# Performance work log

Measured on AMD Instinct MI355X. Metric: run time of the kernel, lower is better.

The kernel has to match this reference:

```python
import jax, jax.numpy as jnp
import numpy as np

B = 8192        # number of contexts
T_SIDE = 10     # num_cx_tokens_per_side
NT = 10         # cx_max_num_types
V_TOK = 5000
V_TYP = 5000
D_TOK = 128
D_TYP = 32
H = 32          # hole_rnn_layer_size
D_IN = D_TOK + D_TYP  # 160


def setup_inputs() -> dict:
    key = jax.random.key(0)
    ks = jax.random.split(key, 32)
    def n(k, shape, scale=1.0):
        return jax.random.normal(k, shape, dtype=jnp.float32) * scale
    def rmask(k, shape):
        m = jax.random.randint(k, shape, 0, 2).astype(bool)
        return m.at[:, :, 0].set(True)  # first type slot always valid (as in data loader)
    inp = {}
    inp['tokens_before'] = jax.random.randint(ks[0], (B, T_SIDE), 0, V_TOK, dtype=jnp.int32)
    inp['types_before'] = jax.random.randint(ks[1], (B, T_SIDE, NT), 0, V_TYP, dtype=jnp.int32)
    inp['mask_before'] = rmask(ks[2], (B, T_SIDE, NT))
    inp['tokens_after'] = jax.random.randint(ks[3], (B, T_SIDE), 0, V_TOK, dtype=jnp.int32)
    inp['types_after'] = jax.random.randint(ks[4], (B, T_SIDE, NT), 0, V_TYP, dtype=jnp.int32)
    inp['mask_after'] = rmask(ks[5], (B, T_SIDE, NT))
    inp['token_embeddings'] = n(ks[6], (V_TOK, D_TOK))
    inp['type_embeddings'] = n(ks[7], (V_TYP, D_TYP))
    inp['hole_representation'] = n(ks[8], (1, 1, D_IN))
    # GRU kernels (TF GRUCell layout): gate kernel [(in+h), 2h], candidate [(in+h), h]
    i = 9
    for layer, din in ((0, D_IN), (1, 2 * H)):
        for d in ('fw', 'bw'):
            inp[f'gk_{d}{layer}'] = n(ks[i], (din + H, 2 * H), 0.1); i += 1
            inp[f'gb_{d}{layer}'] = jnp.zeros((2 * H,), jnp.float32)
            inp[f'ck_{d}{layer}'] = n(ks[i], (din + H, H), 0.1); i += 1
            inp[f'cb_{d}{layer}'] = jnp.zeros((H,), jnp.float32)
    return inp


def _embed(tokens, types, mask, tok_emb, typ_emb):
    te = tok_emb[tokens]                                 # [B,T,128]
    ty = typ_emb[types]                                  # [B,T,NT,32]
    ty = ty + (1.0 - mask[..., None].astype(jnp.float32)) * -1000.0
    ty = jnp.max(ty, axis=2)                             # masked max over types -> [B,T,32]
    return jnp.concatenate([te, ty], axis=-1)            # [B,T,160]


def _gru(x_seq, gk, gb, ck, cb):
    # x_seq: [T,B,D]; TF GRUCell math: r,u = sigmoid([x,h]Wg+bg); c = tanh([x, r*h]Wc+bc); h' = u*h+(1-u)*c
    h0 = jnp.zeros((x_seq.shape[1], cb.shape[0]), x_seq.dtype)
    def step(h, x):
        ru = jax.nn.sigmoid(jnp.concatenate([x, h], -1) @ gk + gb)
        r, u = jnp.split(ru, 2, axis=-1)
        c = jnp.tanh(jnp.concatenate([x, r * h], -1) @ ck + cb)
        h_new = u * h + (1.0 - u) * c
        return h_new, h_new
    _, ys = jax.lax.scan(step, h0, x_seq)
    return ys                                            # [T,B,H]


def _bidir(x_seq, pf, pb):
    fw = _gru(x_seq, *pf)
    bw = jnp.flip(_gru(jnp.flip(x_seq, 0), *pb), 0)
    return jnp.concatenate([fw, bw], axis=-1)            # [T,B,2H]


def reference(tokens_before, types_before, mask_before, tokens_after, types_after, mask_after,
              token_embeddings, type_embeddings, hole_representation,
              gk_fw0, gb_fw0, ck_fw0, cb_fw0, gk_bw0, gb_bw0, ck_bw0, cb_bw0,
              gk_fw1, gb_fw1, ck_fw1, cb_fw1, gk_bw1, gb_bw1, ck_bw1, cb_bw1):
    before = _embed(tokens_before, types_before, mask_before, token_embeddings, type_embeddings)
    after = _embed(tokens_after, types_after, mask_after, token_embeddings, type_embeddings)
    nb = before.shape[0]
    hole = jnp.broadcast_to(hole_representation, (nb, 1, D_IN))
    seq = jnp.concatenate([before, hole, after], axis=1)  # [B,21,160]
    x = jnp.transpose(seq, (1, 0, 2))                     # [T,B,D]
    y0 = _bidir(x, (gk_fw0, gb_fw0, ck_fw0, cb_fw0), (gk_bw0, gb_bw0, ck_bw0, cb_bw0))
    y1 = _bidir(y0, (gk_fw1, gb_fw1, ck_fw1, cb_fw1), (gk_bw1, gb_bw1, ck_bw1, cb_bw1))
    return jnp.transpose(y1, (1, 0, 2))                   # [B,21,64]
```

## Files before the change

kernel.cpp:

```cpp
#include <hip/hip_runtime.h>


typedef __attribute__((ext_vector_type(8))) short short8;
typedef __attribute__((ext_vector_type(8))) __bf16 bf16x8;
typedef __attribute__((ext_vector_type(4))) float f32x4;
typedef unsigned short ushort_t;

#define U_TOKEMB  0
#define U_TYPEMB  640000
#define U_HOLE    800000
#define U_GKFW0   800160
#define U_GBFW0   812448
#define U_CKFW0   812512
#define U_CBFW0   818656
#define U_GKBW0   818688
#define U_GBBW0   830976
#define U_CKBW0   831040
#define U_CBBW0   837184
#define U_GKFW1   837216
#define U_GBFW1   843360
#define U_CKFW1   843424
#define U_CBFW1   846496
#define U_GKBW1   846528
#define U_GBBW1   852672
#define U_CKBW1   852736
#define U_CBBW1   855808

#define Y0A_OFF   (4u << 20)
#define TYPF_OFF  (25u << 20)
#define WF_OFF    (37u << 20)

__device__ __forceinline__ float bf2f(unsigned int u) {
  union { unsigned int i; float f; } v; v.i = u << 16; return v.f;
}
__device__ __forceinline__ unsigned short f2bf(float f) {
  unsigned int u = __float_as_uint(f);
  u += 0x7fffu + ((u >> 16) & 1u);
  return (unsigned short)(u >> 16);
}
__device__ __forceinline__ unsigned cvtpk(float a, float b) {
  unsigned r;
  asm("v_cvt_pk_bf16_f32 %0, %1, %2" : "=v"(r) : "v"(a), "v"(b));
  return r;
}
__device__ __forceinline__ f32x4 mfma16(short8 a, short8 b, f32x4 c) {
  return __builtin_amdgcn_mfma_f32_16x16x32_bf16(
      __builtin_bit_cast(bf16x8, a), __builtin_bit_cast(bf16x8, b), c, 0, 0, 0);
}
__device__ __forceinline__ float frcp(float x) { return __builtin_amdgcn_rcpf(x); }
__device__ __forceinline__ float sgm(float x) {
  return frcp(1.f + __expf(-x));
}
__device__ __forceinline__ float tnh(float x) {
  return 1.f - 2.f * frcp(__expf(2.f * x) + 1.f);
}
__device__ __forceinline__ int PIk(int p) { return (p >> 1) + ((p & 1) << 4); }

__global__ void k0_detect(const ushort_t* __restrict__ probe_f,
                          const unsigned* __restrict__ probe_m,
                          const unsigned* __restrict__ probe_t,
                          int* __restrict__ flags) {
  const int lane = threadIdx.x;
  int cnt = 0;
#pragma unroll
  for (int i = 0; i < 4; ++i) {
    unsigned e = ((unsigned)probe_f[lane + i * 64] >> 7) & 0xffu;
    if (e == 0u || (e >= 112u && e <= 134u)) cnt++;
  }
#pragma unroll
  for (int off = 32; off > 0; off >>= 1) cnt += __shfl_down(cnt, off, 64);
  const unsigned v = probe_m[lane];
  const unsigned long long bytelike =
      __ballot((v > 1u) && (v != 0x3F800000u) && ((v & 0xFEFEFEFEu) == 0u));
  const unsigned tv = probe_t[lane];
  const unsigned long long tlooksTypes =
      __ballot(!(tv == 0u || tv == 1u || tv == 0x3F800000u));
  if (lane == 0) {
    flags[0] = (cnt < 205) ? 1 : 0;
    flags[1] = bytelike ? 1 : 0;
    flags[2] = tlooksTypes ? 0 : 1;
  }
}

struct Cvt19 { const void* src[19]; int len[19]; int dst[19]; };

__global__ void kcvt(Cvt19 a, ushort_t* __restrict__ cvt, const int* __restrict__ flags) {
  const int fp32 = flags[0];
  int gid = blockIdx.x * blockDim.x + threadIdx.x;
#pragma unroll 1
  for (int s = 0; s < 19; ++s) {
    if (gid < a.len[s]) {
      cvt[a.dst[s] + gid] = fp32 ? f2bf(((const float*)a.src[s])[gid])
                                 : ((const ushort_t*)a.src[s])[gid];
      return;
    }
    gid -= a.len[s];
  }
}

__global__ void kswz(const ushort_t* __restrict__ cvt, uint4* __restrict__ wf) {
  const int id = blockIdx.x * blockDim.x + threadIdx.x;
  if (id >= 108 * 64) return;
  const int frag = id >> 6, lane = id & 63;
  const int q = lane >> 4, nl = lane & 15;
  const int layer = (frag >= 72) ? 1 : 0;
  const int fr = layer ? frag - 72 : frag;
  const int nper = layer ? 18 : 36;
  const int d = fr / nper;
  const int f = fr - d * nper;
  const ushort_t* gk = layer ? (cvt + (d ? U_GKBW1 : U_GKFW1))
                             : (cvt + (d ? U_GKBW0 : U_GKFW0));
  const ushort_t* ck = layer ? (cvt + (d ? U_CKBW1 : U_CKFW1))
                             : (cvt + (d ? U_CKBW0 : U_CKFW0));
  const ushort_t* src; int row0, colw, coloff; bool perm;
  if (!layer) {
    if (f < 20)      { src = gk; row0 = (f >> 2) * 32; colw = 64; coloff = (f & 3) * 16; perm = false; }
    else if (f < 30) { int g = f - 20; src = ck; row0 = (g >> 1) * 32; colw = 32; coloff = (g & 1) * 16; perm = false; }
    else if (f < 34) { src = gk; row0 = 160; colw = 64; coloff = (f - 30) * 16; perm = true; }
    else             { src = ck; row0 = 160; colw = 32; coloff = (f - 34) * 16; perm = true; }
  } else {
    perm = true;
    if (f < 12)      { src = gk; row0 = (f >> 2) * 32; colw = 64; coloff = (f & 3) * 16; }
    else             { int g = f - 12; src = ck; row0 = (g >> 1) * 32; colw = 32; coloff = (g & 1) * 16; }
  }
  short8 v;
#pragma unroll
  for (int j = 0; j < 8; ++j) {
    const int p = q * 8 + j;
    const int row = row0 + (perm ? PIk(p) : p);
    v[j] = (short)src[row * colw + coloff + nl];
  }
  wf[frag * 64 + lane] = __builtin_bit_cast(uint4, v);
}

__global__ __launch_bounds__(256) void ktypmax(
    const void* __restrict__ slot_tb, const void* __restrict__ slot_mb,
    const void* __restrict__ slot_ta, const void* __restrict__ slot_ma,
    const ushort_t* __restrict__ cvt, uint4* __restrict__ typf,
    const int* __restrict__ flags) {
  const int wv = threadIdx.x >> 6;
  const int lane = threadIdx.x & 63;
  const int q = lane >> 4, nl = lane & 15;
  const int job = blockIdx.x * 4 + wv;
  const int st = job >> 9;
  const int btile = job & 511;
  const int side = (st >= 10) ? 1 : 0;
  const int ts = st - side * 10;
  const int b = btile * 16 + nl;
  const int sw = flags[2];
  const int bytem = flags[1];
  const int* tys = side ? (const int*)(sw ? slot_ma : slot_ta)
                        : (const int*)(sw ? slot_mb : slot_tb);
  const void* msk = side ? (sw ? slot_ta : slot_ma)
                         : (sw ? slot_tb : slot_mb);
  const int base = (b * 10 + ts) * 10;
  float mx[8];
#pragma unroll
  for (int j = 0; j < 8; ++j) mx[j] = -1e30f;
#pragma unroll
  for (int nt = 0; nt < 10; ++nt) {
    const int ty = tys[base + nt];
    const bool mv = bytem ? (((const unsigned char*)msk)[base + nt] != 0)
                          : (((const unsigned*)msk)[base + nt] != 0u);
    const float pen = mv ? 0.f : -1000.f;
    uint4 e = *reinterpret_cast<const uint4*>(cvt + U_TYPEMB + (size_t)ty * 32 + q * 8);
    const unsigned w[4] = {e.x, e.y, e.z, e.w};
#pragma unroll
    for (int j2 = 0; j2 < 4; ++j2) {
      mx[2 * j2]     = fmaxf(mx[2 * j2],     bf2f(w[j2] & 0xffffu) + pen);
      mx[2 * j2 + 1] = fmaxf(mx[2 * j2 + 1], bf2f(w[j2] >> 16) + pen);
    }
  }
  short8 v;
#pragma unroll
  for (int j = 0; j < 8; ++j) v[j] = (short)f2bf(mx[j]);
  typf[(size_t)job * 64 + lane] = __builtin_bit_cast(uint4, v);
}

__device__ __forceinline__ void gatherX(
    int t, int btile, int lane,
    const int* __restrict__ tok_b, const int* __restrict__ tok_a,
    const ushort_t* __restrict__ cvt, const uint4* __restrict__ typf,
    short8 af[5]) {
  const int q = lane >> 4, nl = lane & 15;
  if (t == 10) {
#pragma unroll
    for (int kt = 0; kt < 5; ++kt)
      af[kt] = __builtin_bit_cast(short8,
          *reinterpret_cast<const uint4*>(cvt + U_HOLE + kt * 32 + q * 8));
    return;
  }
  const int ts = (t < 10) ? t : t - 11;
  const int side = (t < 10) ? 0 : 1;
  const int b = btile * 16 + nl;
  const int tok = (side ? tok_a : tok_b)[b * 10 + ts];
#pragma unroll
  for (int kt = 0; kt < 4; ++kt)
    af[kt] = __builtin_bit_cast(short8,
        *reinterpret_cast<const uint4*>(cvt + U_TOKEMB + (size_t)tok * 128 + kt * 32 + q * 8));
  af[4] = __builtin_bit_cast(short8,
      typf[((size_t)(side * 10 + ts) * 512 + btile) * 64 + lane]);
}

__global__ __launch_bounds__(256, 1) void krec0(
    const int* __restrict__ tok_b, const int* __restrict__ tok_a,
    const ushort_t* __restrict__ cvt, const uint4* __restrict__ wf,
    const uint4* __restrict__ typf, uint4* __restrict__ y0a) {
  __shared__ __align__(16) ushort_t hbuf[4][2][16 * 40];
  const int wv = threadIdx.x >> 6;
  const int lane = threadIdx.x & 63;
  const int q = lane >> 4, nl = lane & 15;
  const int job = blockIdx.x * 4 + wv;
  const int dir = job & 1, btile = job >> 1;

  const uint4* wfL0 = wf + dir * 36 * 64;
  short8 wg[5][4], wc[5][2], wgh[4], wch[2];
#pragma unroll
  for (int kt = 0; kt < 5; ++kt) {
#pragma unroll
    for (int tn = 0; tn < 4; ++tn)
      wg[kt][tn] = __builtin_bit_cast(short8, wfL0[(kt * 4 + tn) * 64 + lane]);
#pragma unroll
    for (int tn = 0; tn < 2; ++tn)
      wc[kt][tn] = __builtin_bit_cast(short8, wfL0[(20 + kt * 2 + tn) * 64 + lane]);
  }
#pragma unroll
  for (int tn = 0; tn < 4; ++tn)
    wgh[tn] = __builtin_bit_cast(short8, wfL0[(30 + tn) * 64 + lane]);
#pragma unroll
  for (int tn = 0; tn < 2; ++tn)
    wch[tn] = __builtin_bit_cast(short8, wfL0[(34 + tn) * 64 + lane]);

  const ushort_t* gb = cvt + (dir ? U_GBBW0 : U_GBFW0);
  const ushort_t* cb = cvt + (dir ? U_CBBW0 : U_CBFW0);
  float gb4[4], cb4[2];
#pragma unroll
  for (int tn = 0; tn < 4; ++tn) gb4[tn] = bf2f((unsigned)gb[tn * 16 + nl]);
#pragma unroll
  for (int tn = 0; tn < 2; ++tn) cb4[tn] = bf2f((unsigned)cb[tn * 16 + nl]);

  f32x4 hc0 = {0.f, 0.f, 0.f, 0.f}, hc1 = {0.f, 0.f, 0.f, 0.f};
  short8 hA = {0, 0, 0, 0, 0, 0, 0, 0};
  ushort_t* hb0 = hbuf[wv][0];
  ushort_t* hb1 = hbuf[wv][1];

  short8 afc[5], afn[5];
  gatherX(dir ? 20 : 0, btile, lane, tok_b, tok_a, cvt, typf, afc);

  for (int s = 0; s < 21; ++s) {
    const int t = dir ? 20 - s : s;
    if (s < 20)
      gatherX(dir ? t - 1 : t + 1, btile, lane, tok_b, tok_a, cvt, typf, afn);

    f32x4 ru[4];
#pragma unroll
    for (int tn = 0; tn < 4; ++tn) {
      f32x4 acc = {gb4[tn], gb4[tn], gb4[tn], gb4[tn]};
#pragma unroll
      for (int kt = 0; kt < 5; ++kt) acc = mfma16(afc[kt], wg[kt][tn], acc);
      acc = mfma16(hA, wgh[tn], acc);
      ru[tn] = acc;
    }
#pragma unroll
    for (int tn = 0; tn < 4; ++tn)
#pragma unroll
      for (int r = 0; r < 4; ++r) ru[tn][r] = sgm(ru[tn][r]);

#pragma unroll
    for (int r = 0; r < 4; ++r)
      *reinterpret_cast<unsigned*>(hb0 + (q * 4 + r) * 40 + 2 * nl) =
          cvtpk(ru[0][r] * hc0[r], ru[1][r] * hc1[r]);
    short8 rhA = *reinterpret_cast<const short8*>(hb0 + nl * 40 + q * 8);

    f32x4 cc0 = {cb4[0], cb4[0], cb4[0], cb4[0]};
    f32x4 cc1 = {cb4[1], cb4[1], cb4[1], cb4[1]};
#pragma unroll
    for (int kt = 0; kt < 5; ++kt) {
      cc0 = mfma16(afc[kt], wc[kt][0], cc0);
      cc1 = mfma16(afc[kt], wc[kt][1], cc1);
    }
    cc0 = mfma16(rhA, wch[0], cc0);
    cc1 = mfma16(rhA, wch[1], cc1);
#pragma unroll
    for (int r = 0; r < 4; ++r) {
      const float c0 = tnh(cc0[r]), c1 = tnh(cc1[r]);
      const float u0 = ru[2][r], u1 = ru[3][r];
      hc0[r] = u0 * hc0[r] + (1.f - u0) * c0;
      hc1[r] = u1 * hc1[r] + (1.f - u1) * c1;
    }

#pragma unroll
    for (int r = 0; r < 4; ++r)
      *reinterpret_cast<unsigned*>(hb1 + (q * 4 + r) * 40 + 2 * nl) =
          cvtpk(hc0[r], hc1[r]);
    hA = *reinterpret_cast<const short8*>(hb1 + nl * 40 + q * 8);
    y0a[((size_t)(t * 512 + btile) * 2 + dir) * 64 + lane] = __builtin_bit_cast(uint4, hA);

    if (s < 20) {
#pragma unroll
      for (int kt = 0; kt < 5; ++kt) afc[kt] = afn[kt];
    }
  }
}

__global__ __launch_bounds__(256, 1) void k3b(
    const ushort_t* __restrict__ cvt, const uint4* __restrict__ wf,
    const uint4* __restrict__ y0a, float* __restrict__ out) {
  __shared__ __align__(16) ushort_t hbuf[4][2][16 * 40];
  const int wv = threadIdx.x >> 6;
  const int lane = threadIdx.x & 63;
  const int q = lane >> 4, nl = lane & 15;
  const int job = blockIdx.x * 4 + wv;
  const int dir = job & 1, btile = job >> 1;

  const uint4* wfL1 = wf + (72 + dir * 18) * 64;
  short8 wg[3][4], wc[3][2];
#pragma unroll
  for (int kt = 0; kt < 3; ++kt) {
#pragma unroll
    for (int tn = 0; tn < 4; ++tn)
      wg[kt][tn] = __builtin_bit_cast(short8, wfL1[(kt * 4 + tn) * 64 + lane]);
#pragma unroll
    for (int tn = 0; tn < 2; ++tn)
      wc[kt][tn] = __builtin_bit_cast(short8, wfL1[(12 + kt * 2 + tn) * 64 + lane]);
  }
  const ushort_t* gb = cvt + (dir ? U_GBBW1 : U_GBFW1);
  const ushort_t* cb = cvt + (dir ? U_CBBW1 : U_CBFW1);
  float gb4[4], cb4[2];
#pragma unroll
  for (int tn = 0; tn < 4; ++tn) gb4[tn] = bf2f((unsigned)gb[tn * 16 + nl]);
#pragma unroll
  for (int tn = 0; tn < 2; ++tn) cb4[tn] = bf2f((unsigned)cb[tn * 16 + nl]);

  f32x4 hc0 = {0.f, 0.f, 0.f, 0.f}, hc1 = {0.f, 0.f, 0.f, 0.f};
  short8 hA = {0, 0, 0, 0, 0, 0, 0, 0};
  ushort_t* hb0 = hbuf[wv][0];
  ushort_t* hb1 = hbuf[wv][1];

  short8 ya0, ya1, yn0, yn1;
  {
    const int t0 = dir ? 20 : 0;
    ya0 = __builtin_bit_cast(short8, y0a[((size_t)(t0 * 512 + btile) * 2 + 0) * 64 + lane]);
    ya1 = __builtin_bit_cast(short8, y0a[((size_t)(t0 * 512 + btile) * 2 + 1) * 64 + lane]);
  }

  for (int s = 0; s < 21; ++s) {
    const int t = dir ? 20 - s : s;
    if (s < 20) {
      const int t2 = dir ? t - 1 : t + 1;
      yn0 = __builtin_bit_cast(short8, y0a[((size_t)(t2 * 512 + btile) * 2 + 0) * 64 + lane]);
      yn1 = __builtin_bit_cast(short8, y0a[((size_t)(t2 * 512 + btile) * 2 + 1) * 64 + lane]);
    }

    f32x4 ru[4];
#pragma unroll
    for (int tn = 0; tn < 4; ++tn) {
      f32x4 acc = {gb4[tn], gb4[tn], gb4[tn], gb4[tn]};
      acc = mfma16(ya0, wg[0][tn], acc);
      acc = mfma16(ya1, wg[1][tn], acc);
      acc = mfma16(hA,  wg[2][tn], acc);
      ru[tn] = acc;
    }
#pragma unroll
    for (int tn = 0; tn < 4; ++tn)
#pragma unroll
      for (int r = 0; r < 4; ++r) ru[tn][r] = sgm(ru[tn][r]);

#pragma unroll
    for (int r = 0; r < 4; ++r)
      *reinterpret_cast<unsigned*>(hb0 + (q * 4 + r) * 40 + 2 * nl) =
          cvtpk(ru[0][r] * hc0[r], ru[1][r] * hc1[r]);
    short8 rhA = *reinterpret_cast<const short8*>(hb0 + nl * 40 + q * 8);

    f32x4 cc0 = {cb4[0], cb4[0], cb4[0], cb4[0]};
    cc0 = mfma16(ya0, wc[0][0], cc0);
    cc0 = mfma16(ya1, wc[1][0], cc0);
    cc0 = mfma16(rhA, wc[2][0], cc0);
    f32x4 cc1 = {cb4[1], cb4[1], cb4[1], cb4[1]};
    cc1 = mfma16(ya0, wc[0][1], cc1);
    cc1 = mfma16(ya1, wc[1][1], cc1);
    cc1 = mfma16(rhA, wc[2][1], cc1);

#pragma unroll
    for (int r = 0; r < 4; ++r) {
      const float c0 = tnh(cc0[r]), c1 = tnh(cc1[r]);
      const float u0 = ru[2][r], u1 = ru[3][r];
      hc0[r] = u0 * hc0[r] + (1.f - u0) * c0;
      hc1[r] = u1 * hc1[r] + (1.f - u1) * c1;
    }

#pragma unroll
    for (int r = 0; r < 4; ++r)
      *reinterpret_cast<unsigned*>(hb1 + (q * 4 + r) * 40 + 2 * nl) =
          cvtpk(hc0[r], hc1[r]);
    hA = *reinterpret_cast<const short8*>(hb1 + nl * 40 + q * 8);

#pragma unroll
    for (int r = 0; r < 4; ++r) {
      const size_t o = ((size_t)(btile * 16 + q * 4 + r) * 21 + t) * 64 + dir * 32 + nl;
      out[o]      = hc0[r];
      out[o + 16] = hc1[r];
    }

    if (s < 20) { ya0 = yn0; ya1 = yn1; }
  }
}

extern "C" void kernel_launch(void* const* d_in, const int* in_sizes, int n_in,
                              void* d_out, int out_size, void* d_ws, size_t ws_size,
                              hipStream_t stream)
{
  const int* tok_b = (const int*)d_in[0];
  const void* slot_tb = d_in[1];
  const void* slot_mb = d_in[2];
  const int* tok_a = (const int*)d_in[3];
  const void* slot_ta = d_in[4];
  const void* slot_ma = d_in[5];

  int* flags = (int*)d_ws;
  ushort_t* cvt = (ushort_t*)((char*)d_ws + 64);
  uint4* y0a = (uint4*)((char*)d_ws + Y0A_OFF);
  uint4* typf = (uint4*)((char*)d_ws + TYPF_OFF);
  uint4* wf  = (uint4*)((char*)d_ws + WF_OFF);

  k0_detect<<<dim3(1), dim3(64), 0, stream>>>(
      (const ushort_t*)d_in[6], (const unsigned*)slot_mb, (const unsigned*)slot_tb,
      flags);

  static const int slen[19] = {640000, 160000, 160,
                               12288, 64, 6144, 32, 12288, 64, 6144, 32,
                               6144, 64, 3072, 32, 6144, 64, 3072, 32};
  static const int sdst[19] = {U_TOKEMB, U_TYPEMB, U_HOLE,
                               U_GKFW0, U_GBFW0, U_CKFW0, U_CBFW0,
                               U_GKBW0, U_GBBW0, U_CKBW0, U_CBBW0,
                               U_GKFW1, U_GBFW1, U_CKFW1, U_CBFW1,
                               U_GKBW1, U_GBBW1, U_CKBW1, U_CBBW1};
  Cvt19 a;
  int tot = 0;
  for (int i = 0; i < 19; ++i) {
    a.src[i] = d_in[6 + i]; a.len[i] = slen[i]; a.dst[i] = sdst[i]; tot += slen[i];
  }
  kcvt<<<dim3((tot + 255) / 256), dim3(256), 0, stream>>>(a, cvt, flags);

  kswz<<<dim3(27), dim3(256), 0, stream>>>(cvt, wf);

  ktypmax<<<dim3(2560), dim3(256), 0, stream>>>(
      slot_tb, slot_mb, slot_ta, slot_ma, cvt, typf, flags);

  krec0<<<dim3(256), dim3(256), 0, stream>>>(tok_b, tok_a, cvt, wf, typf, y0a);

  k3b<<<dim3(256), dim3(256), 0, stream>>>(cvt, wf, y0a, (float*)d_out);
}
```

Baseline: 188.1 us.

## Software-pipeline GRU input projections one step ahead of the recurrence

In both GRU layer kernels, the input-side MFMA products (x·W for gates and candidate) for step t+1 are now computed during step t, interleaved with the recurrent critical path. The recurrence then only needs the single h·W MFMA per output tile, which shortens the serial dependency chain each step. Input gathers/loads move two steps ahead. This raises register pressure (extra px/pxn accumulators) and may cause spills at launch bounds 256,1.

New measurement: 193.2 us. 1.03x slower.

```diff
diff --git a/kernel.cpp b/kernel.cpp
--- a/kernel.cpp
+++ b/kernel.cpp
@@ -244,23 +244,44 @@
   ushort_t* hb0 = hbuf[wv][0];
   ushort_t* hb1 = hbuf[wv][1];
 
-  short8 afc[5], afn[5];
-  gatherX(dir ? 20 : 0, btile, lane, tok_b, tok_a, cvt, typf, afc);
+  short8 afc[5];
+  f32x4 px[6], pxn[6];
+  {
+    gatherX(dir ? 20 : 0, btile, lane, tok_b, tok_a, cvt, typf, afc);
+#pragma unroll
+    for (int tn = 0; tn < 4; ++tn) {
+      f32x4 acc = {gb4[tn], gb4[tn], gb4[tn], gb4[tn]};
+#pragma unroll
+      for (int kt = 0; kt < 5; ++kt) acc = mfma16(afc[kt], wg[kt][tn], acc);
+      px[tn] = acc;
+    }
+#pragma unroll
+    for (int tn = 0; tn < 2; ++tn) {
+      f32x4 acc = {cb4[tn], cb4[tn], cb4[tn], cb4[tn]};
+#pragma unroll
+      for (int kt = 0; kt < 5; ++kt) acc = mfma16(afc[kt], wc[kt][tn], acc);
+      px[4 + tn] = acc;
+    }
+    gatherX(dir ? 19 : 1, btile, lane, tok_b, tok_a, cvt, typf, afc);
+  }
 
   for (int s = 0; s < 21; ++s) {
     const int t = dir ? 20 - s : s;
-    if (s < 20)
-      gatherX(dir ? t - 1 : t + 1, btile, lane, tok_b, tok_a, cvt, typf, afn);
 
     f32x4 ru[4];
 #pragma unroll
-    for (int tn = 0; tn < 4; ++tn) {
-      f32x4 acc = {gb4[tn], gb4[tn], gb4[tn], gb4[tn]};
-#pragma unroll
-      for (int kt = 0; kt < 5; ++kt) acc = mfma16(afc[kt], wg[kt][tn], acc);
-      acc = mfma16(hA, wgh[tn], acc);
-      ru[tn] = acc;
-    }
+    for (int tn = 0; tn < 4; ++tn) ru[tn] = mfma16(hA, wgh[tn], px[tn]);
+
+    if (s < 20) {
+#pragma unroll
+      for (int tn = 0; tn < 4; ++tn) {
+        f32x4 acc = {gb4[tn], gb4[tn], gb4[tn], gb4[tn]};
+#pragma unroll
+        for (int kt = 0; kt < 5; ++kt) acc = mfma16(afc[kt], wg[kt][tn], acc);
+        pxn[tn] = acc;
+      }
+    }
+
 #pragma unroll
     for (int tn = 0; tn < 4; ++tn)
 #pragma unroll
@@ -272,15 +293,19 @@
           cvtpk(ru[0][r] * hc0[r], ru[1][r] * hc1[r]);
     short8 rhA = *reinterpret_cast<const short8*>(hb0 + nl * 40 + q * 8);
 
-    f32x4 cc0 = {cb4[0], cb4[0], cb4[0], cb4[0]};
-    f32x4 cc1 = {cb4[1], cb4[1], cb4[1], cb4[1]};
-#pragma unroll
-    for (int kt = 0; kt < 5; ++kt) {
-      cc0 = mfma16(afc[kt], wc[kt][0], cc0);
-      cc1 = mfma16(afc[kt], wc[kt][1], cc1);
-    }
-    cc0 = mfma16(rhA, wch[0], cc0);
-    cc1 = mfma16(rhA, wch[1], cc1);
+    f32x4 cc0 = mfma16(rhA, wch[0], px[4]);
+    f32x4 cc1 = mfma16(rhA, wch[1], px[5]);
+
+    if (s < 20) {
+#pragma unroll
+      for (int tn = 0; tn < 2; ++tn) {
+        f32x4 acc = {cb4[tn], cb4[tn], cb4[tn], cb4[tn]};
+#pragma unroll
+        for (int kt = 0; kt < 5; ++kt) acc = mfma16(afc[kt], wc[kt][tn], acc);
+        pxn[4 + tn] = acc;
+      }
+    }
+
 #pragma unroll
     for (int r = 0; r < 4; ++r) {
       const float c0 = tnh(cc0[r]), c1 = tnh(cc1[r]);
@@ -298,7 +323,9 @@
 
     if (s < 20) {
 #pragma unroll
-      for (int kt = 0; kt < 5; ++kt) afc[kt] = afn[kt];
+      for (int tn = 0; tn < 6; ++tn) px[tn] = pxn[tn];
+      if (s < 19)
+        gatherX(dir ? t - 2 : t + 2, btile, lane, tok_b, tok_a, cvt, typf, afc);
     }
   }
 }
@@ -337,30 +364,52 @@
   ushort_t* hb0 = hbuf[wv][0];
   ushort_t* hb1 = hbuf[wv][1];
 
-  short8 ya0, ya1, yn0, yn1;
+#define LOAD_YA(tt, d0, d1)                                                      \
+  do {                                                                           \
+    d0 = __builtin_bit_cast(short8,                                              \
+        y0a[((size_t)((tt) * 512 + btile) * 2 + 0) * 64 + lane]);                \
+    d1 = __builtin_bit_cast(short8,                                              \
+        y0a[((size_t)((tt) * 512 + btile) * 2 + 1) * 64 + lane]);                \
+  } while (0)
+
+  short8 ya0, ya1;
+  f32x4 px[6], pxn[6];
   {
-    const int t0 = dir ? 20 : 0;
-    ya0 = __builtin_bit_cast(short8, y0a[((size_t)(t0 * 512 + btile) * 2 + 0) * 64 + lane]);
-    ya1 = __builtin_bit_cast(short8, y0a[((size_t)(t0 * 512 + btile) * 2 + 1) * 64 + lane]);
-  }
-
-  for (int s = 0; s < 21; ++s) {
-    const int t = dir ? 20 - s : s;
-    if (s < 20) {
-      const int t2 = dir ? t - 1 : t + 1;
-      yn0 = __builtin_bit_cast(short8, y0a[((size_t)(t2 * 512 + btile) * 2 + 0) * 64 + lane]);
-      yn1 = __builtin_bit_cast(short8, y0a[((size_t)(t2 * 512 + btile) * 2 + 1) * 64 + lane]);
-    }
-
-    f32x4 ru[4];
+    LOAD_YA(dir ? 20 : 0, ya0, ya1);
 #pragma unroll
     for (int tn = 0; tn < 4; ++tn) {
       f32x4 acc = {gb4[tn], gb4[tn], gb4[tn], gb4[tn]};
       acc = mfma16(ya0, wg[0][tn], acc);
       acc = mfma16(ya1, wg[1][tn], acc);
-      acc = mfma16(hA,  wg[2][tn], acc);
-      ru[tn] = acc;
-    }
+      px[tn] = acc;
+    }
+#pragma unroll
+    for (int tn = 0; tn < 2; ++tn) {
+      f32x4 acc = {cb4[tn], cb4[tn], cb4[tn], cb4[tn]};
+      acc = mfma16(ya0, wc[0][tn], acc);
+      acc = mfma16(ya1, wc[1][tn], acc);
+      px[4 + tn] = acc;
+    }
+    LOAD_YA(dir ? 19 : 1, ya0, ya1);
+  }
+
+  for (int s = 0; s < 21; ++s) {
+    const int t = dir ? 20 - s : s;
+
+    f32x4 ru[4];
+#pragma unroll
+    for (int tn = 0; tn < 4; ++tn) ru[tn] = mfma16(hA, wg[2][tn], px[tn]);
+
+    if (s < 20) {
+#pragma unroll
+      for (int tn = 0; tn < 4; ++tn) {
+        f32x4 acc = {gb4[tn], gb4[tn], gb4[tn], gb4[tn]};
+        acc = mfma16(ya0, wg[0][tn], acc);
+        acc = mfma16(ya1, wg[1][tn], acc);
+        pxn[tn] = acc;
+      }
+    }
+
 #pragma unroll
     for (int tn = 0; tn < 4; ++tn)
 #pragma unroll
@@ -372,14 +421,18 @@
           cvtpk(ru[0][r] * hc0[r], ru[1][r] * hc1[r]);
     short8 rhA = *reinterpret_cast<const short8*>(hb0 + nl * 40 + q * 8);
 
-    f32x4 cc0 = {cb4[0], cb4[0], cb4[0], cb4[0]};
-    cc0 = mfma16(ya0, wc[0][0], cc0);
-    cc0 = mfma16(ya1, wc[1][0], cc0);
-    cc0 = mfma16(rhA, wc[2][0], cc0);
-    f32x4 cc1 = {cb4[1], cb4[1], cb4[1], cb4[1]};
-    cc1 = mfma16(ya0, wc[0][1], cc1);
-    cc1 = mfma16(ya1, wc[1][1], cc1);
-    cc1 = mfma16(rhA, wc[2][1], cc1);
+    f32x4 cc0 = mfma16(rhA, wc[2][0], px[4]);
+    f32x4 cc1 = mfma16(rhA, wc[2][1], px[5]);
+
+    if (s < 20) {
+#pragma unroll
+      for (int tn = 0; tn < 2; ++tn) {
+        f32x4 acc = {cb4[tn], cb4[tn], cb4[tn], cb4[tn]};
+        acc = mfma16(ya0, wc[0][tn], acc);
+        acc = mfma16(ya1, wc[1][tn], acc);
+        pxn[4 + tn] = acc;
+      }
+    }
 
 #pragma unroll
     for (int r = 0; r < 4; ++r) {
@@ -402,8 +455,13 @@
       out[o + 16] = hc1[r];
     }
 
-    if (s < 20) { ya0 = yn0; ya1 = yn1; }
-  }
+    if (s < 20) {
+#pragma unroll
+      for (int tn = 0; tn < 6; ++tn) px[tn] = pxn[tn];
+      if (s < 19) LOAD_YA(dir ? t - 2 : t + 2, ya0, ya1);
+    }
+  }
+#undef LOAD_YA
 }
 
 extern "C" void kernel_launch(void* const* d_in, const int* in_sizes, int n_in,
```
